# Performance work log

Measured on AMD Instinct MI355X. Metric: run time of the kernel, lower is better.

## Reference

```python
import jax, jax.numpy as jnp
import numpy as np

# ---- db4 filters (pywt conventions: dec_lo = rec_lo[::-1], rec_hi = qmf(rec_lo)) ----
F = 8  # db4 filter length
_rec_lo = np.array([0.23037781330885523, 0.7148465705525415, 0.6308807679295904,
                    -0.027983769416983849, -0.18703481171888114, 0.030841381835986965,
                    0.032883011666982945, -0.010597401784997278], dtype=np.float32)
_rec_hi = _rec_lo[::-1].copy()
_rec_hi[1::2] *= -1.0
REC_LO = jnp.asarray(_rec_lo)
REC_HI = jnp.asarray(_rec_hi)

MAX_LEVEL = 9  # pywt.dwt_max_level(4096, 8)


def _conv1d(x, kernel, stride=1, padding='VALID', lhs_dilation=None):
    # x: [B, L] -> correlation (XLA conv does NOT flip the kernel)
    out = jax.lax.conv_general_dilated(
        x[:, None, :], kernel[None, None, :],
        window_strides=(stride,), padding=padding,
        lhs_dilation=lhs_dilation,
        dimension_numbers=('NCH', 'OIH', 'NCH'))
    return out[:, 0, :]


def dwt(x):
    # pywt.dwt(x, 'db4', mode='symmetric'):
    # cA = np.convolve(sym_ext(x, F-1), dec_lo, 'valid')[1::2]
    # convolution with dec filter == correlation with rec filter (its reverse)
    ext = jnp.pad(x, ((0, 0), (F - 1, F - 1)), mode='symmetric')[:, 1:]
    return _conv1d(ext, REC_LO, stride=2), _conv1d(ext, REC_HI, stride=2)


def idwt(ca, cd):
    # pywt.idwt: zero-upsample coeffs, full convolution with rec filters, trim edges
    n = ca.shape[1]
    pad = ((F - 1, F - 1),)
    out = (_conv1d(ca, REC_LO[::-1], padding=pad, lhs_dilation=(2,)) +
           _conv1d(cd, REC_HI[::-1], padding=pad, lhs_dilation=(2,)))
    return out[:, F - 2:2 * n]  # output length = 2n - F + 2


def wavelet_features(x1):
    # Faithful to WaveletDWTLayer stack + WaveletParsingLayer: at each level k>=2,
    # reconstruct with details of levels k and k-1 only (others zeroed), with
    # pywt.waverec's trim-by-one rule; concatenate the 8 full-length reconstructions.
    a = x1
    cds, recs = [], []
    for level in range(1, MAX_LEVEL + 1):
        a, d = dwt(a)
        if level >= 2:
            r = idwt(jnp.zeros_like(d), d)
            for j in range(level - 2, -1, -1):
                dj = cds[j] if j == level - 2 else jnp.zeros_like(cds[j])
                if r.shape[1] == dj.shape[1] + 1:  # waverec trim rule
                    r = r[:, :-1]
                r = idwt(r, dj)
            recs.append(r)  # [B, signal_length]
        cds.append(d)
    return jnp.concatenate(recs, axis=1)  # [B, signal_length*(MAX_LEVEL-1)]


def reference(x1, x2, x3, W0, b0, W1, b1, W2, b2):
    # x2/x3 are placeholders in the original module (overwritten by layers 1/2)
    h = wavelet_features(x1)
    for W, b in ((W0, b0), (W1, b1), (W2, b2)):
        h = jax.nn.relu(h) @ W.T + b
    return h


def setup_inputs() -> dict:
    key = jax.random.key(0)
    ks = jax.random.split(key, 4)
    B, N = 2048, 4096
    D_IN, H1, H2, OUT = 32768, 181, 13, 10
    return {
        'x1': jax.random.normal(ks[0], (B, N), jnp.float32),
        'x2': jnp.zeros((B, 1, 8), jnp.float32),
        'x3': jnp.zeros((B, 1, 8), jnp.float32),
        'W0': jax.random.normal(ks[1], (H1, D_IN), jnp.float32) / np.float32(np.sqrt(D_IN)),
        'b0': jnp.zeros((H1,), jnp.float32),
        'W1': jax.random.normal(ks[2], (H2, H1), jnp.float32) / np.float32(np.sqrt(H1)),
        'b1': jnp.zeros((H2,), jnp.float32),
        'W2': jax.random.normal(ks[3], (OUT, H2), jnp.float32) / np.float32(np.sqrt(H2)),
        'b2': jnp.zeros((OUT,), jnp.float32),
    }
```

## Files before the change

kernel.cpp:

```cpp
#include <hip/hip_runtime.h>
#include <hip/hip_bf16.h>


typedef _Float16 f16x8 __attribute__((ext_vector_type(8)));
typedef _Float16 f16x4v __attribute__((ext_vector_type(4)));
typedef float f32x4 __attribute__((ext_vector_type(4)));

#define WV_THREADS 256
#define DROW 4144
#define NSPLIT 16
#define KCHUNK 2048

#define L0 0.23037781330885523f
#define L1 0.7148465705525415f
#define L2f 0.6308807679295904f
#define L3 -0.02798376941698385f
#define L4 -0.18703481171888114f
#define L5 0.030841381835986965f
#define L6 0.032883011666982945f
#define L7 -0.010597401784997278f

#define H0 -0.010597401784997278f
#define H1 -0.032883011666982945f
#define H2 0.030841381835986965f
#define H3 0.18703481171888114f
#define H4 -0.02798376941698385f
#define H5 -0.6308807679295904f
#define H6 0.7148465705525415f
#define H7 -0.23037781330885523f

__device__ __forceinline__ int ext_idx(int j, int n) {
  return (j < 6) ? (5 - j) : ((j < n + 6) ? (j - 6) : (2 * n + 5 - j));
}

__device__ __forceinline__ void dwt2(const float* a, float* anext, float* d,
                                     int n, int m, bool store_a) {
  const int ng = (m + 1) >> 1;
  for (int g = threadIdx.x; g < ng; g += WV_THREADS) {
    float w[10];
    if (g >= 2 && 4 * g + 9 <= n + 5) {
      const float2* af = (const float2*)a + (2 * g - 3);
      float2 b0 = af[0], b1 = af[1], b2 = af[2], b3 = af[3], b4 = af[4];
      w[0] = b0.x; w[1] = b0.y; w[2] = b1.x; w[3] = b1.y; w[4] = b2.x;
      w[5] = b2.y; w[6] = b3.x; w[7] = b3.y; w[8] = b4.x; w[9] = b4.y;
    } else {
#pragma unroll
      for (int q = 0; q < 10; ++q) {
        int j = 4 * g + q;
        int jm = n + 12;
        if (j > jm) j = jm;
        w[q] = a[ext_idx(j, n)];
      }
    }
    float sl0 = w[0]*L0 + w[1]*L1 + w[2]*L2f + w[3]*L3 + w[4]*L4 + w[5]*L5 + w[6]*L6 + w[7]*L7;
    float sh0 = w[0]*H0 + w[1]*H1 + w[2]*H2  + w[3]*H3 + w[4]*H4 + w[5]*H5 + w[6]*H6 + w[7]*H7;
    float sl1 = w[2]*L0 + w[3]*L1 + w[4]*L2f + w[5]*L3 + w[6]*L4 + w[7]*L5 + w[8]*L6 + w[9]*L7;
    float sh1 = w[2]*H0 + w[3]*H1 + w[4]*H2  + w[5]*H3 + w[6]*H4 + w[7]*H5 + w[8]*H6 + w[9]*H7;
    if (2 * g + 1 < m) {
      if (store_a) *(float2*)(anext + 2 * g) = make_float2(sl0, sl1);
      *(float2*)(d + 2 * g) = make_float2(sh0, sh1);
    } else {
      if (store_a) anext[2 * g] = sl0;
      d[2 * g] = sh0;
    }
  }
}

template <bool HAS_CA, bool HAS_CD, bool FINAL>
__device__ __forceinline__ void idwt2(const float* ca, const float* cd,
                                      float* outl, _Float16* outg, int dlen) {
  const int npair = dlen - 3;
  const int ng = (npair + 1) >> 1;
  for (int g = threadIdx.x; g < ng; g += WV_THREADS) {
    float e0 = 0.f, o0 = 0.f, e1 = 0.f, o1 = 0.f;
    if (HAS_CA) {
      const float2* f = (const float2*)ca + g;
      float2 a0 = f[0], a1 = f[1], a2 = f[2];
      e0 = a1.y*L0 + a1.x*L2f + a0.y*L4 + a0.x*L6;
      o0 = a1.y*L1 + a1.x*L3  + a0.y*L5 + a0.x*L7;
      e1 = a2.x*L0 + a1.y*L2f + a1.x*L4 + a0.y*L6;
      o1 = a2.x*L1 + a1.y*L3  + a1.x*L5 + a0.y*L7;
    }
    if (HAS_CD) {
      const float2* f = (const float2*)cd + g;
      float2 d0 = f[0], d1 = f[1], d2 = f[2];
      e0 += d1.y*H0 + d1.x*H2 + d0.y*H4 + d0.x*H6;
      o0 += d1.y*H1 + d1.x*H3 + d0.y*H5 + d0.x*H7;
      e1 += d2.x*H0 + d1.y*H2 + d1.x*H4 + d0.y*H6;
      o1 += d2.x*H1 + d1.y*H3 + d1.x*H5 + d0.y*H7;
    }
    bool full = (2 * g + 1 < npair);
    if (FINAL) {
      if (full) {
        f16x4v h;
        h[0] = (_Float16)fmaxf(e0, 0.f); h[1] = (_Float16)fmaxf(o0, 0.f);
        h[2] = (_Float16)fmaxf(e1, 0.f); h[3] = (_Float16)fmaxf(o1, 0.f);
        *(f16x4v*)(outg + 4 * g) = h;
      } else {
        outg[4 * g]     = (_Float16)fmaxf(e0, 0.f);
        outg[4 * g + 1] = (_Float16)fmaxf(o0, 0.f);
      }
    } else {
      if (full) *(float4*)(outl + 4 * g) = make_float4(e0, o0, e1, o1);
      else      *(float2*)(outl + 4 * g) = make_float2(e0, o0);
    }
  }
}

__global__ __launch_bounds__(WV_THREADS) void wv_analysis_cvt(
    const float* __restrict__ x, float* __restrict__ dG,
    const float* __restrict__ W0, _Float16* __restrict__ Bw) {
  __shared__ float r1[4104];
  __shared__ float r2[2056];
  const int tid = threadIdx.x;

  if (blockIdx.x >= 2048) {
    size_t i = ((size_t)(blockIdx.x - 2048) * 256 + tid) * 4;
    int rowc = (int)(i >> 15);
    f16x4v h;
    if (rowc < 181) {
      const float4 v = *(const float4*)(W0 + i);
      h[0] = (_Float16)v.x; h[1] = (_Float16)v.y;
      h[2] = (_Float16)v.z; h[3] = (_Float16)v.w;
    } else {
      h[0] = (_Float16)0.f; h[1] = (_Float16)0.f;
      h[2] = (_Float16)0.f; h[3] = (_Float16)0.f;
    }
    *(f16x4v*)(Bw + i) = h;
    return;
  }

  const int NLa[10]  = {4096, 2051, 1029, 518, 262, 134, 70, 38, 22, 14};
  const int DOFF[10] = {0, 0, 2052, 3082, 3600, 3862, 3996, 4066, 4104, 4126};
  const int LOFF[10] = {0, 0, 1036, 520, 2068, 1040, 2332, 1176, 2404, 1216};
  const int row = blockIdx.x;

  const float4* xr = (const float4*)(x + (size_t)row * 4096);
  for (int i = tid; i < 1024; i += WV_THREADS) ((float4*)r1)[i] = xr[i];
  __syncthreads();

  float* dr = dG + (size_t)row * DROW;
  dwt2(r1, r2, dr + DOFF[1], NLa[0], NLa[1], true);
  __syncthreads();
  const float* ap = r2;
  float* an = r1;
  for (int lev = 2; lev <= 9; ++lev) {
    float* dbuf = ((lev & 1) ? r2 : r1) + LOFF[lev];
    dwt2(ap, an, dbuf, NLa[lev - 1], NLa[lev], lev < 9);
    __syncthreads();
    const float* t = ap; ap = an; an = (float*)t;
  }
  for (int lev = 2; lev <= 9; ++lev) {
    const float* src = ((lev & 1) ? r2 : r1) + LOFF[lev];
    float* dst = dr + DOFF[lev];
    const int n = NLa[lev];
    for (int i = 2 * tid; i + 1 < n; i += 2 * WV_THREADS)
      *(float2*)(dst + i) = *(const float2*)(src + i);
    if ((n & 1) && tid == 0) dst[n - 1] = src[n - 1];
  }
}

__global__ __launch_bounds__(WV_THREADS, 6) void wv_synth(
    const float* __restrict__ dG, _Float16* __restrict__ A) {
  __shared__ float s1[2052];
  __shared__ float s2[2052];
  const int NLa[10]  = {4096, 2051, 1029, 518, 262, 134, 70, 38, 22, 14};
  const int DOFF[10] = {0, 0, 2052, 3082, 3600, 3862, 3996, 4066, 4104, 4126};
  const int row = blockIdx.x;
  const int L = 2 + blockIdx.y;
  const float* dr = dG + (size_t)row * DROW;

  idwt2<false, true, false>(nullptr, dr + DOFF[L], s1, nullptr, NLa[L]);
  __syncthreads();
  float* cur = s1;
  float* nxt = s2;
  for (int j = L - 2; j >= 1; --j) {
    if (j == L - 2)
      idwt2<true, true, false>(cur, dr + DOFF[j + 1], nxt, nullptr, NLa[j + 1]);
    else
      idwt2<true, false, false>(cur, nullptr, nxt, nullptr, NLa[j + 1]);
    __syncthreads();
    float* t = cur; cur = nxt; nxt = t;
  }
  _Float16* og = A + (size_t)row * 32768 + (size_t)(L - 2) * 4096;
  if (L == 2)
    idwt2<true, true, true>(cur, dr + DOFF[1], nullptr, og, 2051);
  else
    idwt2<true, false, true>(cur, nullptr, nullptr, og, 2051);
}

__device__ __forceinline__ void load_lds16(const void* g, void* l) {
  __builtin_amdgcn_global_load_lds((__attribute__((address_space(1))) unsigned int*)g,
                                   (__attribute__((address_space(3))) unsigned int*)l,
                                   16, 0, 0);
}

__global__ __launch_bounds__(256, 2) void gemm_kernel(
    const _Float16* __restrict__ A, const _Float16* __restrict__ Bw,
    float* __restrict__ P) {
  __shared__ _Float16 As[128 * 64];
  __shared__ _Float16 Bs[192 * 64];
  const int tid = threadIdx.x;
  const int lane = tid & 63;
  const int wave = tid >> 6;
  const int id = blockIdx.x;
  const int k_idx = (id & 7) + 8 * ((id >> 3) >> 4);
  const int m_idx = (id >> 3) & 15;
  const int m0 = m_idx * 128;
  const int k0 = k_idx * KCHUNK;

  f32x4 acc[2][12];
#pragma unroll
  for (int mt = 0; mt < 2; ++mt)
#pragma unroll
    for (int nt = 0; nt < 12; ++nt) acc[mt][nt] = (f32x4){0.f, 0.f, 0.f, 0.f};

  for (int ks = 0; ks < (KCHUNK >> 6); ++ks) {
    const int kbase = k0 + (ks << 6);
    __syncthreads();
#pragma unroll
    for (int t = 0; t < 4; ++t) {
      int g = ((wave * 4 + t) << 6) + lane;
      int r = g >> 3, cs = g & 7;
      const _Float16* gp = A + (size_t)(m0 + r) * 32768 + kbase + ((cs ^ (r & 7)) << 3);
      load_lds16(gp, (char*)As + (size_t)((wave * 4 + t) << 10));
    }
#pragma unroll
    for (int t = 0; t < 6; ++t) {
      int g = ((wave * 6 + t) << 6) + lane;
      int r = g >> 3, cs = g & 7;
      const _Float16* gp = Bw + (size_t)r * 32768 + kbase + ((cs ^ (r & 7)) << 3);
      load_lds16(gp, (char*)Bs + (size_t)((wave * 6 + t) << 10));
    }
    __syncthreads();
#pragma unroll
    for (int kk = 0; kk < 2; ++kk) {
      const int chunk = kk * 4 + (lane >> 4);
      f16x8 af[2];
#pragma unroll
      for (int mt = 0; mt < 2; ++mt) {
        int r = wave * 32 + mt * 16 + (lane & 15);
        af[mt] = *(const f16x8*)(As + r * 64 + ((chunk ^ (r & 7)) << 3));
      }
#pragma unroll
      for (int nt = 0; nt < 12; ++nt) {
        int rb = nt * 16 + (lane & 15);
        f16x8 bf = *(const f16x8*)(Bs + rb * 64 + ((chunk ^ (rb & 7)) << 3));
        acc[0][nt] = __builtin_amdgcn_mfma_f32_16x16x32_f16(af[0], bf, acc[0][nt], 0, 0, 0);
        acc[1][nt] = __builtin_amdgcn_mfma_f32_16x16x32_f16(af[1], bf, acc[1][nt], 0, 0, 0);
      }
    }
  }
  float* Pp = P + ((size_t)k_idx * 2048 + m0) * 192;
#pragma unroll
  for (int mt = 0; mt < 2; ++mt)
#pragma unroll
    for (int nt = 0; nt < 12; ++nt)
#pragma unroll
      for (int r4 = 0; r4 < 4; ++r4) {
        int rr = wave * 32 + mt * 16 + ((lane >> 4) << 2) + r4;
        int cc = nt * 16 + (lane & 15);
        Pp[(size_t)rr * 192 + cc] = acc[mt][nt][r4];
      }
}

__global__ __launch_bounds__(256) void mlp_kernel(
    const float* __restrict__ P, const float* __restrict__ b0,
    const float* __restrict__ W1, const float* __restrict__ b1,
    const float* __restrict__ W2, const float* __restrict__ b2,
    float* __restrict__ out) {
  __shared__ float part[4][193];
  __shared__ float h1[192];
  __shared__ float h2[13];
  const int row = blockIdx.x;
  const int t = threadIdx.x;
  const int g = t >> 6;
  const int l = t & 63;

  float a0 = 0.f, a1 = 0.f, a2 = 0.f;
  for (int si = 0; si < NSPLIT / 4; ++si) {
    int s = g + (si << 2);
    const float* Pr = P + ((size_t)s * 2048 + row) * 192;
    a0 += Pr[l]; a1 += Pr[64 + l]; a2 += Pr[128 + l];
  }
  part[g][l] = a0; part[g][64 + l] = a1; part[g][128 + l] = a2;
  __syncthreads();

  if (t < 192) {
    float v = part[0][t] + part[1][t] + part[2][t] + part[3][t];
    h1[t] = (t < 181) ? fmaxf(v + b0[t], 0.f) : 0.f;
  }
  __syncthreads();

#pragma unroll
  for (int r = 0; r < 4; ++r) {
    int j = g + (r << 2);
    if (j < 13) {
      float v = 0.f;
#pragma unroll
      for (int q = 0; q < 3; ++q) {
        int n = l + (q << 6);
        if (n < 181) v += h1[n] * W1[j * 181 + n];
      }
      for (int off = 32; off >= 1; off >>= 1) v += __shfl_down(v, off);
      if (l == 0) h2[j] = fmaxf(v + b1[j], 0.f);
    }
  }
  __syncthreads();

  if (t < 10) {
    float c = b2[t];
#pragma unroll
    for (int j = 0; j < 13; ++j) c += h2[j] * W2[t * 13 + j];
    out[(size_t)row * 10 + t] = c;
  }
}

extern "C" void kernel_launch(void* const* d_in, const int* in_sizes, int n_in,
                              void* d_out, int out_size, void* d_ws, size_t ws_size,
                              hipStream_t stream) {
  const float* x1 = (const float*)d_in[0];
  const float* W0 = (const float*)d_in[3];
  const float* b0 = (const float*)d_in[4];
  const float* W1 = (const float*)d_in[5];
  const float* b1 = (const float*)d_in[6];
  const float* W2 = (const float*)d_in[7];
  const float* b2 = (const float*)d_in[8];
  float* out = (float*)d_out;

  char* ws = (char*)d_ws;
  const size_t A_BYTES = (size_t)2048 * 32768 * 2;
  const size_t B_BYTES = (size_t)192 * 32768 * 2;
  _Float16* Afeat = (_Float16*)ws;
  _Float16* Bw = (_Float16*)(ws + A_BYTES);
  float* Dq = (float*)(ws + A_BYTES + B_BYTES);
  float* P = (float*)(ws + A_BYTES + B_BYTES);

  wv_analysis_cvt<<<2048 + 6144, WV_THREADS, 0, stream>>>(x1, Dq, W0, Bw);
  dim3 sg(2048, 8);
  wv_synth<<<sg, WV_THREADS, 0, stream>>>(Dq, Afeat);
  gemm_kernel<<<16 * NSPLIT, 256, 0, stream>>>(Afeat, Bw, P);
  mlp_kernel<<<2048, 256, 0, stream>>>(P, b0, W1, b1, W2, b2, out);
}
```

Measured before the change: 243.1 us.

## Specialize wavelet synthesis per level and double GEMM split-K count

Rewrites the synthesis stage so each level's cascade is a compile-time template with constant lengths, fully unrolled per-thread loops and no runtime-indexed tables. The GEMM split-K goes from 16 to 32 chunks of 1024, giving 512 blocks instead of 256 to fill more CUs, with a 2D grid replacing the old block-index swizzle. The extra partial sums mean more P traffic and more reduction work in the MLP kernel, and dropping the swizzle can change L2 locality. This assumes the partial buffer and the MLP reduction already size themselves from NSPLIT.

```diff
diff --git a/kernel.cpp b/kernel.cpp
--- a/kernel.cpp
+++ b/kernel.cpp
@@ -8,8 +8,8 @@
 
 #define WV_THREADS 256
 #define DROW 4144
-#define NSPLIT 16
-#define KCHUNK 2048
+#define NSPLIT 32
+#define KCHUNK 1024
 
 #define L0 0.23037781330885523f
 #define L1 0.7148465705525415f
@@ -28,6 +28,9 @@
 #define H5 -0.6308807679295904f
 #define H6 0.7148465705525415f
 #define H7 -0.23037781330885523f
+
+__constant__ constexpr int cNL[10]   = {4096, 2051, 1029, 518, 262, 134, 70, 38, 22, 14};
+__constant__ constexpr int cDOFF[10] = {0, 0, 2052, 3082, 3600, 3862, 3996, 4066, 4104, 4126};
 
 __device__ __forceinline__ int ext_idx(int j, int n) {
   return (j < 6) ? (5 - j) : ((j < n + 6) ? (j - 6) : (2 * n + 5 - j));
@@ -66,45 +69,79 @@
   }
 }
 
-template <bool HAS_CA, bool HAS_CD, bool FINAL>
-__device__ __forceinline__ void idwt2(const float* ca, const float* cd,
-                                      float* outl, _Float16* outg, int dlen) {
-  const int npair = dlen - 3;
-  const int ng = (npair + 1) >> 1;
-  for (int g = threadIdx.x; g < ng; g += WV_THREADS) {
-    float e0 = 0.f, o0 = 0.f, e1 = 0.f, o1 = 0.f;
-    if (HAS_CA) {
-      const float2* f = (const float2*)ca + g;
-      float2 a0 = f[0], a1 = f[1], a2 = f[2];
-      e0 = a1.y*L0 + a1.x*L2f + a0.y*L4 + a0.x*L6;
-      o0 = a1.y*L1 + a1.x*L3  + a0.y*L5 + a0.x*L7;
-      e1 = a2.x*L0 + a1.y*L2f + a1.x*L4 + a0.y*L6;
-      o1 = a2.x*L1 + a1.y*L3  + a1.x*L5 + a0.y*L7;
-    }
-    if (HAS_CD) {
-      const float2* f = (const float2*)cd + g;
-      float2 d0 = f[0], d1 = f[1], d2 = f[2];
-      e0 += d1.y*H0 + d1.x*H2 + d0.y*H4 + d0.x*H6;
-      o0 += d1.y*H1 + d1.x*H3 + d0.y*H5 + d0.x*H7;
-      e1 += d2.x*H0 + d1.y*H2 + d1.x*H4 + d0.y*H6;
-      o1 += d2.x*H1 + d1.y*H3 + d1.x*H5 + d0.y*H7;
-    }
-    bool full = (2 * g + 1 < npair);
-    if (FINAL) {
-      if (full) {
-        f16x4v h;
-        h[0] = (_Float16)fmaxf(e0, 0.f); h[1] = (_Float16)fmaxf(o0, 0.f);
-        h[2] = (_Float16)fmaxf(e1, 0.f); h[3] = (_Float16)fmaxf(o1, 0.f);
-        *(f16x4v*)(outg + 4 * g) = h;
+template <bool HAS_CA, bool HAS_CD, bool FINAL, int DLEN>
+__device__ __forceinline__ void idwt2t(const float* ca, const float* cd,
+                                       float* outl, _Float16* outg) {
+  constexpr int npair = DLEN - 3;
+  constexpr int ng = (npair + 1) >> 1;
+  constexpr bool clean = (ng % WV_THREADS) == 0;
+#pragma unroll
+  for (int g0 = 0; g0 < ng; g0 += WV_THREADS) {
+    const int g = g0 + (int)threadIdx.x;
+    if (clean || g < ng) {
+      float e0 = 0.f, o0 = 0.f, e1 = 0.f, o1 = 0.f;
+      if (HAS_CA) {
+        const float2* f = (const float2*)ca + g;
+        float2 a0 = f[0], a1 = f[1], a2 = f[2];
+        e0 = a1.y*L0 + a1.x*L2f + a0.y*L4 + a0.x*L6;
+        o0 = a1.y*L1 + a1.x*L3  + a0.y*L5 + a0.x*L7;
+        e1 = a2.x*L0 + a1.y*L2f + a1.x*L4 + a0.y*L6;
+        o1 = a2.x*L1 + a1.y*L3  + a1.x*L5 + a0.y*L7;
+      }
+      if (HAS_CD) {
+        const float2* f = (const float2*)cd + g;
+        float2 d0 = f[0], d1 = f[1], d2 = f[2];
+        e0 += d1.y*H0 + d1.x*H2 + d0.y*H4 + d0.x*H6;
+        o0 += d1.y*H1 + d1.x*H3 + d0.y*H5 + d0.x*H7;
+        e1 += d2.x*H0 + d1.y*H2 + d1.x*H4 + d0.y*H6;
+        o1 += d2.x*H1 + d1.y*H3 + d1.x*H5 + d0.y*H7;
+      }
+      const bool full = (2 * g + 1 < npair);
+      if (FINAL) {
+        if (full) {
+          f16x4v h;
+          h[0] = (_Float16)fmaxf(e0, 0.f); h[1] = (_Float16)fmaxf(o0, 0.f);
+          h[2] = (_Float16)fmaxf(e1, 0.f); h[3] = (_Float16)fmaxf(o1, 0.f);
+          *(f16x4v*)(outg + 4 * g) = h;
+        } else {
+          outg[4 * g]     = (_Float16)fmaxf(e0, 0.f);
+          outg[4 * g + 1] = (_Float16)fmaxf(o0, 0.f);
+        }
       } else {
-        outg[4 * g]     = (_Float16)fmaxf(e0, 0.f);
-        outg[4 * g + 1] = (_Float16)fmaxf(o0, 0.f);
-      }
-    } else {
-      if (full) *(float4*)(outl + 4 * g) = make_float4(e0, o0, e1, o1);
-      else      *(float2*)(outl + 4 * g) = make_float2(e0, o0);
-    }
-  }
+        if (full) *(float4*)(outl + 4 * g) = make_float4(e0, o0, e1, o1);
+        else      *(float2*)(outl + 4 * g) = make_float2(e0, o0);
+      }
+    }
+  }
+}
+
+template <int L>
+__device__ __forceinline__ void synth_cascade(const float* dr, _Float16* og,
+                                              float* s1, float* s2) {
+  idwt2t<false, true, false, cNL[L]>(nullptr, dr + cDOFF[L], s1, nullptr);
+  __syncthreads();
+  float* cur = s1;
+  float* nxt = s2;
+  if constexpr (L >= 3) {
+    idwt2t<true, true, false, cNL[L - 1]>(cur, dr + cDOFF[L - 1], nxt, nullptr);
+    __syncthreads();
+    float* t = cur; cur = nxt; nxt = t;
+  }
+#define NOCD_STEP(DL)                                             \
+  {                                                               \
+    idwt2t<true, false, false, DL>(cur, nullptr, nxt, nullptr);   \
+    __syncthreads();                                              \
+    float* t = cur; cur = nxt; nxt = t;                           \
+  }
+  if constexpr (L >= 9) NOCD_STEP(cNL[7])
+  if constexpr (L >= 8) NOCD_STEP(cNL[6])
+  if constexpr (L >= 7) NOCD_STEP(cNL[5])
+  if constexpr (L >= 6) NOCD_STEP(cNL[4])
+  if constexpr (L >= 5) NOCD_STEP(cNL[3])
+  if constexpr (L >= 4) NOCD_STEP(cNL[2])
+#undef NOCD_STEP
+  idwt2t<true, (L == 2), true, 2051>(cur, (L == 2) ? dr + cDOFF[1] : nullptr,
+                                     nullptr, og);
 }
 
 __global__ __launch_bounds__(WV_THREADS) void wv_analysis_cvt(
@@ -164,29 +201,19 @@
     const float* __restrict__ dG, _Float16* __restrict__ A) {
   __shared__ float s1[2052];
   __shared__ float s2[2052];
-  const int NLa[10]  = {4096, 2051, 1029, 518, 262, 134, 70, 38, 22, 14};
-  const int DOFF[10] = {0, 0, 2052, 3082, 3600, 3862, 3996, 4066, 4104, 4126};
   const int row = blockIdx.x;
-  const int L = 2 + blockIdx.y;
   const float* dr = dG + (size_t)row * DROW;
-
-  idwt2<false, true, false>(nullptr, dr + DOFF[L], s1, nullptr, NLa[L]);
-  __syncthreads();
-  float* cur = s1;
-  float* nxt = s2;
-  for (int j = L - 2; j >= 1; --j) {
-    if (j == L - 2)
-      idwt2<true, true, false>(cur, dr + DOFF[j + 1], nxt, nullptr, NLa[j + 1]);
-    else
-      idwt2<true, false, false>(cur, nullptr, nxt, nullptr, NLa[j + 1]);
-    __syncthreads();
-    float* t = cur; cur = nxt; nxt = t;
-  }
-  _Float16* og = A + (size_t)row * 32768 + (size_t)(L - 2) * 4096;
-  if (L == 2)
-    idwt2<true, true, true>(cur, dr + DOFF[1], nullptr, og, 2051);
-  else
-    idwt2<true, false, true>(cur, nullptr, nullptr, og, 2051);
+  _Float16* og = A + (size_t)row * 32768 + (size_t)blockIdx.y * 4096;
+  switch (blockIdx.y) {
+    case 0: synth_cascade<2>(dr, og, s1, s2); break;
+    case 1: synth_cascade<3>(dr, og, s1, s2); break;
+    case 2: synth_cascade<4>(dr, og, s1, s2); break;
+    case 3: synth_cascade<5>(dr, og, s1, s2); break;
+    case 4: synth_cascade<6>(dr, og, s1, s2); break;
+    case 5: synth_cascade<7>(dr, og, s1, s2); break;
+    case 6: synth_cascade<8>(dr, og, s1, s2); break;
+    default: synth_cascade<9>(dr, og, s1, s2); break;
+  }
 }
 
 __device__ __forceinline__ void load_lds16(const void* g, void* l) {
@@ -203,10 +230,8 @@
   const int tid = threadIdx.x;
   const int lane = tid & 63;
   const int wave = tid >> 6;
-  const int id = blockIdx.x;
-  const int k_idx = (id & 7) + 8 * ((id >> 3) >> 4);
-  const int m_idx = (id >> 3) & 15;
-  const int m0 = m_idx * 128;
+  const int m0 = blockIdx.x * 128;
+  const int k_idx = blockIdx.y;
   const int k0 = k_idx * KCHUNK;
 
   f32x4 acc[2][12];
@@ -339,6 +364,7 @@
   wv_analysis_cvt<<<2048 + 6144, WV_THREADS, 0, stream>>>(x1, Dq, W0, Bw);
   dim3 sg(2048, 8);
   wv_synth<<<sg, WV_THREADS, 0, stream>>>(Dq, Afeat);
-  gemm_kernel<<<16 * NSPLIT, 256, 0, stream>>>(Afeat, Bw, P);
+  dim3 gg(16, NSPLIT);
+  gemm_kernel<<<gg, 256, 0, stream>>>(Afeat, Bw, P);
   mlp_kernel<<<2048, 256, 0, stream>>>(P, b0, W1, b1, W2, b2, out);
 }
```

Result: faster. 217.4 us (-10.6%).
